# Performance work log

Measured on AMD Instinct MI355X. Metric: run time of the kernel, lower is better.

## Reference

```python
import jax, jax.numpy as jnp
import numpy as np

BS, T, N = 16, 50, 100
OBS, ACT, HID, LAT = 40, 8, 64, 16
NEG = -9e15


def _gat(x, adj, w, a_src, a_dst, b, concat, alpha=0.2):
    # x: [B, n, fin]; w: [H, fin, fout]
    h = jnp.einsum('bni,hio->bhno', x, w)
    e_src = jnp.einsum('bhno,ho->bhn', h, a_src[..., 0])
    e_dst = jnp.einsum('bhno,ho->bhn', h, a_dst[..., 0])
    e = e_src[:, :, :, None] + e_dst[:, :, None, :]        # [B,H,n,n]
    e = jnp.where(e > 0, e, alpha * e)                     # LeakyReLU
    e = jnp.where(adj[None, None] > 0, e, NEG)             # mask by adjacency
    att = jax.nn.softmax(e, axis=-1)
    hp = jnp.einsum('bhnm,bhmo->bhno', att, h)
    if concat:
        B, H, n, fo = hp.shape
        return jax.nn.elu(hp.transpose(0, 2, 1, 3).reshape(B, n, H * fo) + b)
    return hp.mean(axis=1) + b


def _lstm(x, Wih, Whh, bih, bhh):
    # x: [B, T, H]; PyTorch gate order i, f, g, o
    def step(carry, xt):
        h, c = carry
        g = xt @ Wih + h @ Whh + bih + bhh
        i, f, gg, o = jnp.split(g, 4, axis=-1)
        c = jax.nn.sigmoid(f) * c + jax.nn.sigmoid(i) * jnp.tanh(gg)
        h = jax.nn.sigmoid(o) * jnp.tanh(c)
        return (h, c), h
    h0 = jnp.zeros((x.shape[0], Whh.shape[0]), x.dtype)
    _, ys = jax.lax.scan(step, (h0, h0), x.transpose(1, 0, 2))
    return ys.transpose(1, 0, 2)


def _forward(o, a_prev, m, eps, params, adj):
    (W_obs, b_obs, W_pa, b_pa, W_mk, b_mk, id_emb,
     lWih, lWhh, lbih, lbhh,
     e1w, e1s, e1d, e1b, e2w, e2s, e2d, e2b,
     d1w, d1s, d1d, d1b, d2w, d2s, d2d, d2b,
     d3w, d3s, d3d, d3b) = params
    bs, t, n, _ = o.shape
    # encode: summed embeddings (dropout is identity in eval)
    emb = (o @ W_obs + b_obs) + (a_prev @ W_pa + b_pa) + (m @ W_mk + b_mk) + id_emb[None, None]
    x = emb.transpose(0, 2, 1, 3).reshape(bs * n, t, HID)
    x = _lstm(x, lWih, lWhh, lbih, lbhh)
    x = x.reshape(bs, n, t, HID).transpose(0, 2, 1, 3).reshape(bs * t, n, HID)
    x = _gat(x, adj, e1w, e1s, e1d, e1b, True)
    x = _gat(x, adj, e2w, e2s, e2d, e2b, False)
    logits = x.reshape(bs, t, n, 2 * LAT).mean(axis=-2)    # AverageGlobalPool over nodes
    mu, logvar = jnp.split(logits, 2, axis=-1)
    z = mu + eps * jnp.exp(0.5 * logvar)                   # reparameterize
    zu = jnp.repeat(z[:, :, None, :], n, axis=2)           # RepeatGlobalUnpool
    d = jnp.concatenate([emb, zu], axis=-1).reshape(bs * t, n, HID + LAT)
    d = _gat(d, adj, d1w, d1s, d1d, d1b, True)
    d = _gat(d, adj, d2w, d2s, d2d, d2b, True)
    d = _gat(d, adj, d3w, d3s, d3d, d3b, False)
    a_recon = d.reshape(bs, t, n, ACT) * m
    return a_recon, mu, logvar


def setup_inputs() -> dict:
    key = jax.random.key(0)
    it = iter(jax.random.split(key, 48))
    def nrm(shape, s=0.1):
        return s * jax.random.normal(next(it), shape, jnp.float32)
    inp = {}
    inp['o'] = jax.random.normal(next(it), (BS, T, N, OBS), jnp.float32)
    inp['a_prev'] = jax.random.uniform(next(it), (BS, T, N, ACT), jnp.float32)
    inp['m'] = (jax.random.uniform(next(it), (BS, T, N, ACT)) > 0.5).astype(jnp.float32)
    inp['eps'] = jax.random.normal(next(it), (BS, T, LAT), jnp.float32)
    adj = jax.random.randint(next(it), (N, N), 0, 2).astype(jnp.int32)
    inp['adj'] = adj.at[jnp.arange(N), jnp.arange(N)].set(1)
    inp['W_obs'] = nrm((OBS, HID)); inp['b_obs'] = jnp.zeros((HID,), jnp.float32)
    inp['W_pa'] = nrm((ACT, HID)); inp['b_pa'] = jnp.zeros((HID,), jnp.float32)
    inp['W_mk'] = nrm((ACT, HID)); inp['b_mk'] = jnp.zeros((HID,), jnp.float32)
    inp['id_emb'] = nrm((N, HID), 1.0)
    inp['lWih'] = nrm((HID, 4 * HID)); inp['lWhh'] = nrm((HID, 4 * HID))
    inp['lbih'] = jnp.zeros((4 * HID,), jnp.float32); inp['lbhh'] = jnp.zeros((4 * HID,), jnp.float32)
    def gat_p(pfx, H, fin, fout, bdim):
        inp[pfx + 'w'] = nrm((H, fin, fout))
        inp[pfx + 's'] = nrm((H, fout, 1))
        inp[pfx + 'd'] = nrm((H, fout, 1))
        inp[pfx + 'b'] = jnp.zeros((bdim,), jnp.float32)
    gat_p('e1', 4, HID, HID // 4, HID)
    gat_p('e2', 1, HID, 2 * LAT, 2 * LAT)
    gat_p('d1', 4, LAT + HID, HID // 4, HID)
    gat_p('d2', 4, HID, HID // 4, HID)
    gat_p('d3', 1, HID, ACT, ACT)
    return inp


def reference(o, a_prev, m, eps, adj, W_obs, b_obs, W_pa, b_pa, W_mk, b_mk, id_emb,
              lWih, lWhh, lbih, lbhh,
              e1w, e1s, e1d, e1b, e2w, e2s, e2d, e2b,
              d1w, d1s, d1d, d1b, d2w, d2s, d2d, d2b,
              d3w, d3s, d3d, d3b):
    params = (W_obs, b_obs, W_pa, b_pa, W_mk, b_mk, id_emb,
              lWih, lWhh, lbih, lbhh,
              e1w, e1s, e1d, e1b, e2w, e2s, e2d, e2b,
              d1w, d1s, d1d, d1b, d2w, d2s, d2d, d2b,
              d3w, d3s, d3d, d3b)
    return _forward(o, a_prev, m, eps, params, adj)
```

## Files before the change

kernel.cpp:

```cpp
#include <hip/hip_runtime.h>

#define BS  16
#define TT  50
#define NN  100
#define OBSF 40
#define ACTF 8
#define HIDF 64
#define LATF 16

__device__ __forceinline__ float sigmf(float x) { return 1.f / (1.f + __expf(-x)); }
__device__ __forceinline__ float tanh_fast(float x) { return 1.f - 2.f / (__expf(2.f * x) + 1.f); }

__global__ void adjmask_kernel(const int* __restrict__ adj, unsigned long long* __restrict__ mask) {
    int n = threadIdx.x;
    if (n < NN) {
        unsigned long long w0 = 0ull, w1 = 0ull;
        for (int m = 0; m < 64; ++m)  if (adj[n * NN + m] > 0) w0 |= (1ull << m);
        for (int m = 64; m < NN; ++m) if (adj[n * NN + m] > 0) w1 |= (1ull << (m - 64));
        mask[2 * n] = w0; mask[2 * n + 1] = w1;
    }
}

__global__ void emb_kernel(const float* __restrict__ o, const float* __restrict__ ap,
                           const float* __restrict__ mk,
                           const float* __restrict__ Wobs, const float* __restrict__ bobs,
                           const float* __restrict__ Wpa, const float* __restrict__ bpa,
                           const float* __restrict__ Wmk, const float* __restrict__ bmk,
                           const float* __restrict__ idemb, float* __restrict__ emb) {
    int g = blockIdx.x;
    int n = g % NN;
    int j = threadIdx.x;
    __shared__ float so[OBSF], sa[ACTF], sm[ACTF];
    if (j < OBSF) so[j] = o[(size_t)g * OBSF + j];
    if (j >= 40 && j < 48) sa[j - 40] = ap[(size_t)g * ACTF + (j - 40)];
    if (j >= 48 && j < 56) sm[j - 48] = mk[(size_t)g * ACTF + (j - 48)];
    __syncthreads();
    float acc = bobs[j] + bpa[j] + bmk[j] + idemb[n * HIDF + j];
    #pragma unroll
    for (int k = 0; k < OBSF; ++k) acc += so[k] * Wobs[k * HIDF + j];
    #pragma unroll
    for (int k = 0; k < ACTF; ++k) acc += sa[k] * Wpa[k * HIDF + j] + sm[k] * Wmk[k * HIDF + j];
    emb[(size_t)g * HIDF + j] = acc;
}

__global__ void xw_kernel(const float* __restrict__ emb, const float* __restrict__ Wih,
                          const float* __restrict__ bih, const float* __restrict__ bhh,
                          float* __restrict__ xW) {
    int blk = blockIdx.x;
    int chunk = blk % 5;
    int s = blk / 5;
    int b = s / NN, n = s % NN;
    int t0 = chunk * 10;
    __shared__ float se[10][HIDF];
    int tid = threadIdx.x;
    for (int i = tid; i < 10 * HIDF; i += 256) {
        int r = i >> 6, k = i & 63;
        se[r][k] = emb[((size_t)(b * TT + t0 + r) * NN + n) * HIDF + k];
    }
    __syncthreads();
    int j = tid;
    float base = bih[j] + bhh[j];
    float acc[10];
    #pragma unroll
    for (int r = 0; r < 10; ++r) acc[r] = base;
    for (int k = 0; k < HIDF; ++k) {
        float w = Wih[k * 256 + j];
        #pragma unroll
        for (int r = 0; r < 10; ++r) acc[r] += se[r][k] * w;
    }
    #pragma unroll
    for (int r = 0; r < 10; ++r) xW[((size_t)s * TT + t0 + r) * 256 + j] = acc[r];
}

__launch_bounds__(256)
__global__ void lstm_kernel(const float* __restrict__ xW, const float* __restrict__ Whh,
                            float* __restrict__ xenc) {
    int s = blockIdx.x;
    int b = s / NN, n = s % NN;
    int j = threadIdx.x;
    __shared__ __align__(16) float hs[HIDF];
    __shared__ float gs[256];
    float wcol[HIDF];
    #pragma unroll
    for (int k = 0; k < HIDF; ++k) wcol[k] = Whh[k * 256 + j];
    if (j < HIDF) hs[j] = 0.f;
    float c = 0.f;
    __syncthreads();
    for (int t = 0; t < TT; ++t) {
        float acc = xW[((size_t)s * TT + t) * 256 + j];
        const float4* h4 = (const float4*)hs;
        #pragma unroll
        for (int k4 = 0; k4 < HIDF / 4; ++k4) {
            float4 hv = h4[k4];
            acc += hv.x * wcol[4 * k4] + hv.y * wcol[4 * k4 + 1]
                 + hv.z * wcol[4 * k4 + 2] + hv.w * wcol[4 * k4 + 3];
        }
        gs[j] = acc;
        __syncthreads();
        if (j < HIDF) {
            float ig = sigmf(gs[j]);
            float fg = sigmf(gs[64 + j]);
            float gg = tanh_fast(gs[128 + j]);
            float og = sigmf(gs[192 + j]);
            c = fg * c + ig * gg;
            float h = og * tanh_fast(c);
            hs[j] = h;
            xenc[((size_t)(b * TT + t) * NN + n) * HIDF + j] = h;
        }
        __syncthreads();
    }
}

template <int FIN1, int FIN2, int H, int FOUT, int SPLIT, int OUTMODE>
__launch_bounds__(256)
__global__ void gat_kernel(const float* __restrict__ x1, const float* __restrict__ x2,
                           const float* __restrict__ w, const float* __restrict__ asrc,
                           const float* __restrict__ adst, const float* __restrict__ bias,
                           const unsigned long long* __restrict__ adjmask,
                           const float* __restrict__ mgate, float* __restrict__ out) {
    constexpr int FIN = FIN1 + FIN2;
    constexpr int HF = H * FOUT;
    constexpr int NPT = 256 / HF;
    constexpr int ROWS = (NN + NPT - 1) / NPT;
    constexpr int SB = NN * (FIN > HF ? FIN : HF);
    __shared__ __align__(16) float sbuf[SB];
    __shared__ __align__(16) float ses[H * NN];
    __shared__ __align__(16) float sed[H * NN];
    __shared__ unsigned long long smask[2 * NN];
    int g = blockIdx.x;
    int tid = threadIdx.x;

    for (int i = tid; i < NN * FIN1; i += 256) {
        int n = i / FIN1, k = i % FIN1;
        sbuf[n * FIN + k] = x1[((size_t)g * NN + n) * FIN1 + k];
    }
    if constexpr (FIN2 > 0) {
        for (int i = tid; i < NN * FIN2; i += 256) {
            int n = i / FIN2, k = i % FIN2;
            sbuf[n * FIN + FIN1 + k] = x2[(size_t)g * FIN2 + k];
        }
    }
    if (tid < 2 * NN) smask[tid] = adjmask[tid];
    __syncthreads();

    const int ho = tid % HF;
    const int h = ho / FOUT, o = ho % FOUT;
    const int n0 = tid / HF;
    float racc[ROWS];
    {
        float wcol[FIN];
        #pragma unroll
        for (int k = 0; k < FIN; ++k) wcol[k] = w[(h * FIN + k) * FOUT + o];
        const float as = asrc[ho], ad = adst[ho];
        #pragma unroll
        for (int r = 0; r < ROWS; ++r) {
            int n = n0 + r * NPT;
            float acc = 0.f;
            if (ROWS * NPT == NN || n < NN) {
                const float4* row = (const float4*)&sbuf[n * FIN];
                #pragma unroll
                for (int k4 = 0; k4 < FIN / 4; ++k4) {
                    float4 xv = row[k4];
                    acc += xv.x * wcol[4 * k4] + xv.y * wcol[4 * k4 + 1]
                         + xv.z * wcol[4 * k4 + 2] + xv.w * wcol[4 * k4 + 3];
                }
            }
            racc[r] = acc;
            float vs = acc * as, vd = acc * ad;
            #pragma unroll
            for (int off = FOUT / 2; off >= 1; off >>= 1) {
                vs += __shfl_xor(vs, off, 64);
                vd += __shfl_xor(vd, off, 64);
            }
            if (o == 0 && (ROWS * NPT == NN || n < NN)) {
                ses[h * NN + n] = vs; sed[h * NN + n] = vd;
            }
        }
    }
    __syncthreads();
    #pragma unroll
    for (int r = 0; r < ROWS; ++r) {
        int n = n0 + r * NPT;
        if (ROWS * NPT == NN || n < NN) sbuf[n * HF + ho] = racc[r];
    }
    __syncthreads();

    constexpr int FT = FOUT / SPLIT;
    constexpr int ITEMS = H * NN * SPLIT;
    for (int idx = tid; idx < ITEMS; idx += 256) {
        int h2 = idx / (NN * SPLIT);
        int rem = idx % (NN * SPLIT);
        int n = rem / SPLIT;
        int os = (rem % SPLIT) * FT;
        unsigned long long m0 = smask[2 * n], m1 = smask[2 * n + 1];
        float esn = ses[h2 * NN + n];
        float denom = 0.f;
        float acc[FT];
        #pragma unroll
        for (int q = 0; q < FT; ++q) acc[q] = 0.f;
        const float4* sed4 = (const float4*)&sed[h2 * NN];
        #pragma unroll 2
        for (int g4 = 0; g4 < NN / 4; ++g4) {
            float4 ev = sed4[g4];
            unsigned int bits = (g4 < 16) ? (unsigned int)(m0 >> (4 * g4))
                                          : (unsigned int)(m1 >> (4 * g4 - 64));
            float e0 = esn + ev.x; e0 = (e0 > 0.f) ? e0 : 0.2f * e0;
            float e1 = esn + ev.y; e1 = (e1 > 0.f) ? e1 : 0.2f * e1;
            float e2 = esn + ev.z; e2 = (e2 > 0.f) ? e2 : 0.2f * e2;
            float e3 = esn + ev.w; e3 = (e3 > 0.f) ? e3 : 0.2f * e3;
            float p0 = (bits & 1u) ? __expf(e0) : 0.f;
            float p1 = (bits & 2u) ? __expf(e1) : 0.f;
            float p2 = (bits & 4u) ? __expf(e2) : 0.f;
            float p3 = (bits & 8u) ? __expf(e3) : 0.f;
            denom += (p0 + p1) + (p2 + p3);
            const float* r0 = &sbuf[(4 * g4 + 0) * HF + h2 * FOUT + os];
            const float* r1 = &sbuf[(4 * g4 + 1) * HF + h2 * FOUT + os];
            const float* r2 = &sbuf[(4 * g4 + 2) * HF + h2 * FOUT + os];
            const float* r3 = &sbuf[(4 * g4 + 3) * HF + h2 * FOUT + os];
            #pragma unroll
            for (int q4 = 0; q4 < FT / 4; ++q4) {
                float4 v0 = ((const float4*)r0)[q4];
                float4 v1 = ((const float4*)r1)[q4];
                float4 v2 = ((const float4*)r2)[q4];
                float4 v3 = ((const float4*)r3)[q4];
                acc[4 * q4 + 0] += p0 * v0.x + p1 * v1.x + p2 * v2.x + p3 * v3.x;
                acc[4 * q4 + 1] += p0 * v0.y + p1 * v1.y + p2 * v2.y + p3 * v3.y;
                acc[4 * q4 + 2] += p0 * v0.z + p1 * v1.z + p2 * v2.z + p3 * v3.z;
                acc[4 * q4 + 3] += p0 * v0.w + p1 * v1.w + p2 * v2.w + p3 * v3.w;
            }
        }
        float inv = 1.f / denom;
        if constexpr (OUTMODE == 0) {
            float4* op = (float4*)&out[((size_t)g * NN + n) * HF + h2 * FOUT + os];
            #pragma unroll
            for (int q4 = 0; q4 < FT / 4; ++q4) {
                float4 v;
                float a0 = acc[4 * q4 + 0] * inv + bias[h2 * FOUT + os + 4 * q4 + 0];
                float a1 = acc[4 * q4 + 1] * inv + bias[h2 * FOUT + os + 4 * q4 + 1];
                float a2 = acc[4 * q4 + 2] * inv + bias[h2 * FOUT + os + 4 * q4 + 2];
                float a3 = acc[4 * q4 + 3] * inv + bias[h2 * FOUT + os + 4 * q4 + 3];
                v.x = (a0 > 0.f) ? a0 : (__expf(a0) - 1.f);
                v.y = (a1 > 0.f) ? a1 : (__expf(a1) - 1.f);
                v.z = (a2 > 0.f) ? a2 : (__expf(a2) - 1.f);
                v.w = (a3 > 0.f) ? a3 : (__expf(a3) - 1.f);
                op[q4] = v;
            }
        } else if constexpr (OUTMODE == 1) {
            float4* op = (float4*)&out[((size_t)g * NN + n) * FOUT + os];
            #pragma unroll
            for (int q4 = 0; q4 < FT / 4; ++q4) {
                float4 v;
                v.x = acc[4 * q4 + 0] * inv + bias[os + 4 * q4 + 0];
                v.y = acc[4 * q4 + 1] * inv + bias[os + 4 * q4 + 1];
                v.z = acc[4 * q4 + 2] * inv + bias[os + 4 * q4 + 2];
                v.w = acc[4 * q4 + 3] * inv + bias[os + 4 * q4 + 3];
                op[q4] = v;
            }
        } else {
            size_t base = ((size_t)g * NN + n) * FOUT + os;
            float4* op = (float4*)&out[base];
            const float4* mp = (const float4*)&mgate[base];
            #pragma unroll
            for (int q4 = 0; q4 < FT / 4; ++q4) {
                float4 mv = mp[q4];
                float4 v;
                v.x = (acc[4 * q4 + 0] * inv + bias[os + 4 * q4 + 0]) * mv.x;
                v.y = (acc[4 * q4 + 1] * inv + bias[os + 4 * q4 + 1]) * mv.y;
                v.z = (acc[4 * q4 + 2] * inv + bias[os + 4 * q4 + 2]) * mv.z;
                v.w = (acc[4 * q4 + 3] * inv + bias[os + 4 * q4 + 3]) * mv.w;
                op[q4] = v;
            }
        }
    }
}

__global__ void pool_kernel(const float* __restrict__ g2, const float* __restrict__ eps,
                            float* __restrict__ z, float* __restrict__ dout) {
    int g = blockIdx.x;
    int c = threadIdx.x;
    __shared__ float s[2 * LATF];
    if (c < 2 * LATF) {
        float sum = 0.f;
        for (int n = 0; n < NN; ++n) sum += g2[((size_t)g * NN + n) * (2 * LATF) + c];
        s[c] = sum * (1.f / NN);
    }
    __syncthreads();
    if (c < LATF) {
        float mu = s[c], lv = s[LATF + c];
        dout[640000 + (size_t)g * LATF + c] = mu;
        dout[652800 + (size_t)g * LATF + c] = lv;
        z[(size_t)g * LATF + c] = mu + eps[(size_t)g * LATF + c] * __expf(0.5f * lv);
    }
}

extern "C" void kernel_launch(void* const* d_in, const int* in_sizes, int n_in,
                              void* d_out, int out_size, void* d_ws, size_t ws_size,
                              hipStream_t stream) {
    const float* o     = (const float*)d_in[0];
    const float* aprev = (const float*)d_in[1];
    const float* mk    = (const float*)d_in[2];
    const float* eps   = (const float*)d_in[3];
    const int*   adj   = (const int*)d_in[4];
    const float* Wobs  = (const float*)d_in[5];
    const float* bobs  = (const float*)d_in[6];
    const float* Wpa   = (const float*)d_in[7];
    const float* bpa   = (const float*)d_in[8];
    const float* Wmk   = (const float*)d_in[9];
    const float* bmk   = (const float*)d_in[10];
    const float* idemb = (const float*)d_in[11];
    const float* lWih  = (const float*)d_in[12];
    const float* lWhh  = (const float*)d_in[13];
    const float* lbih  = (const float*)d_in[14];
    const float* lbhh  = (const float*)d_in[15];
    const float* e1w = (const float*)d_in[16]; const float* e1s = (const float*)d_in[17];
    const float* e1d = (const float*)d_in[18]; const float* e1b = (const float*)d_in[19];
    const float* e2w = (const float*)d_in[20]; const float* e2s = (const float*)d_in[21];
    const float* e2d = (const float*)d_in[22]; const float* e2b = (const float*)d_in[23];
    const float* d1w = (const float*)d_in[24]; const float* d1s = (const float*)d_in[25];
    const float* d1d = (const float*)d_in[26]; const float* d1b = (const float*)d_in[27];
    const float* d2w = (const float*)d_in[28]; const float* d2s = (const float*)d_in[29];
    const float* d2d = (const float*)d_in[30]; const float* d2b = (const float*)d_in[31];
    const float* d3w = (const float*)d_in[32]; const float* d3s = (const float*)d_in[33];
    const float* d3d = (const float*)d_in[34]; const float* d3b = (const float*)d_in[35];

    float* ws   = (float*)d_ws;
    float* emb  = ws;
    float* xenc = ws + 5120000;
    float* xW   = ws + 10240000;
    float* g1o  = ws + 10240000;
    float* g2o  = ws + 15360000;
    float* z    = ws + 17920000;
    float* d1o  = ws + 18000000;
    float* d2o  = ws + 23200000;
    unsigned long long* amask = (unsigned long long*)(ws + 30720000);
    float* out = (float*)d_out;

    adjmask_kernel<<<1, 128, 0, stream>>>(adj, amask);
    emb_kernel<<<BS * TT * NN, 64, 0, stream>>>(o, aprev, mk, Wobs, bobs, Wpa, bpa,
                                                Wmk, bmk, idemb, emb);
    xw_kernel<<<1600 * 5, 256, 0, stream>>>(emb, lWih, lbih, lbhh, xW);
    lstm_kernel<<<1600, 256, 0, stream>>>(xW, lWhh, xenc);
    gat_kernel<64, 0, 4, 16, 1, 0><<<800, 256, 0, stream>>>(xenc, nullptr, e1w, e1s, e1d, e1b,
                                                            amask, nullptr, g1o);
    gat_kernel<64, 0, 1, 32, 4, 1><<<800, 256, 0, stream>>>(g1o, nullptr, e2w, e2s, e2d, e2b,
                                                            amask, nullptr, g2o);
    pool_kernel<<<800, 64, 0, stream>>>(g2o, eps, z, out);
    gat_kernel<64, 16, 4, 16, 1, 0><<<800, 256, 0, stream>>>(emb, z, d1w, d1s, d1d, d1b,
                                                             amask, nullptr, d1o);
    gat_kernel<64, 0, 4, 16, 1, 0><<<800, 256, 0, stream>>>(d1o, nullptr, d2w, d2s, d2d, d2b,
                                                            amask, nullptr, d2o);
    gat_kernel<64, 0, 1, 8, 2, 2><<<800, 256, 0, stream>>>(d2o, nullptr, d3w, d3s, d3d, d3b,
                                                           amask, mk, out);
}
```

Baseline: 590.8 us.

## Run 4-head GAT layers on bf16 MFMA for projection and attention aggregation

Adds a new GAT kernel for the three 4-head layers. It computes the feature projection and the attention-weighted aggregation with 16x16x32 bf16 MFMA instructions instead of scalar FP32 loops. Attention weights are packed to bf16, and the softmax denominator is accumulated from the truncated values so it stays consistent with them. The adjacency mask is also stored as 32-bit words. This trades bf16 precision in the projections and attention weights for matrix-core throughput.

```diff
diff --git a/kernel.cpp b/kernel.cpp
--- a/kernel.cpp
+++ b/kernel.cpp
@@ -8,16 +8,45 @@
 #define HIDF 64
 #define LATF 16
 
+typedef __attribute__((ext_vector_type(8))) short bf16x8;
+typedef __attribute__((ext_vector_type(4))) float f32x4;
+
 __device__ __forceinline__ float sigmf(float x) { return 1.f / (1.f + __expf(-x)); }
 __device__ __forceinline__ float tanh_fast(float x) { return 1.f - 2.f / (__expf(2.f * x) + 1.f); }
 
-__global__ void adjmask_kernel(const int* __restrict__ adj, unsigned long long* __restrict__ mask) {
+__device__ __forceinline__ unsigned bf16pk_rne(float a, float b) {
+    unsigned ua = __float_as_uint(a); ua += 0x7fffu + ((ua >> 16) & 1u);
+    unsigned ub = __float_as_uint(b); ub += 0x7fffu + ((ub >> 16) & 1u);
+    return (ua >> 16) | (ub & 0xffff0000u);
+}
+__device__ __forceinline__ unsigned bf16pk_trunc(float a, float b) {
+    return (__float_as_uint(a) >> 16) | (__float_as_uint(b) & 0xffff0000u);
+}
+__device__ __forceinline__ float bf16trunc_f(float a) {
+    return __uint_as_float(__float_as_uint(a) & 0xffff0000u);
+}
+
+__global__ void adjmask_kernel(const int* __restrict__ adj, unsigned long long* __restrict__ mask,
+                               unsigned* __restrict__ mask32) {
     int n = threadIdx.x;
-    if (n < NN) {
-        unsigned long long w0 = 0ull, w1 = 0ull;
-        for (int m = 0; m < 64; ++m)  if (adj[n * NN + m] > 0) w0 |= (1ull << m);
-        for (int m = 64; m < NN; ++m) if (adj[n * NN + m] > 0) w1 |= (1ull << (m - 64));
-        mask[2 * n] = w0; mask[2 * n + 1] = w1;
+    if (n < 112) {
+        unsigned d0 = 0, d1 = 0, d2 = 0, d3 = 0;
+        if (n < NN) {
+            for (int m = 0; m < NN; ++m) {
+                if (adj[n * NN + m] > 0) {
+                    if (m < 32) d0 |= 1u << m;
+                    else if (m < 64) d1 |= 1u << (m - 32);
+                    else if (m < 96) d2 |= 1u << (m - 64);
+                    else d3 |= 1u << (m - 96);
+                }
+            }
+        }
+        mask32[n * 4 + 0] = d0; mask32[n * 4 + 1] = d1;
+        mask32[n * 4 + 2] = d2; mask32[n * 4 + 3] = d3;
+        if (n < NN) {
+            mask[2 * n] = (unsigned long long)d0 | ((unsigned long long)d1 << 32);
+            mask[2 * n + 1] = (unsigned long long)d2 | ((unsigned long long)d3 << 32);
+        }
     }
 }
 
@@ -108,6 +137,179 @@
             xenc[((size_t)(b * TT + t) * NN + n) * HIDF + j] = h;
         }
         __syncthreads();
+    }
+}
+
+template <int FIN1, int FIN2>
+__launch_bounds__(256)
+__global__ void gat4_mfma_kernel(const float* __restrict__ x1, const float* __restrict__ x2,
+                                 const float* __restrict__ w, const float* __restrict__ asrc,
+                                 const float* __restrict__ adst, const float* __restrict__ bias,
+                                 const unsigned* __restrict__ mask32, float* __restrict__ out) {
+    constexpr int FIN = FIN1 + FIN2;
+    constexpr int FINP = (FIN + 31) & ~31;
+    constexpr int KC1 = FINP / 32;
+    constexpr int SXP = FINP + 8;
+    constexpr int SWP = FINP + 8;
+    constexpr int SH2P = 136;
+    constexpr int R1A = 112 * SXP * 2;
+    constexpr int R1B = 4 * 16 * SH2P * 2;
+    constexpr int R1 = (R1A > R1B) ? R1A : R1B;
+    constexpr int R2A = 64 * SWP * 2;
+    constexpr int R2B = (448 + 512 + 448 + 448) * 4;
+    constexpr int R2 = (R2A > R2B) ? R2A : R2B;
+    __shared__ __align__(16) char smem[R1 + R2];
+    short* sxa = (short*)smem;
+    short* sh2 = (short*)smem;
+    short* swb = (short*)(smem + R1);
+    float* ses = (float*)(smem + R1);
+    float* sed = ses + 448;
+    float* sden = sed + 512;
+    unsigned* smk = (unsigned*)(sden + 448);
+
+    const int g = blockIdx.x, tid = threadIdx.x;
+    const int wv = tid >> 6, lane = tid & 63, q = lane >> 4, c = lane & 15;
+    const int head = wv;
+
+    for (int i = tid; i < 112 * (SXP / 2); i += 256) {
+        int n = i / (SXP / 2), k2 = i % (SXP / 2);
+        int k = 2 * k2;
+        float lo = 0.f, hi = 0.f;
+        if (n < NN) {
+            if (k < FIN1) {
+                float2 v = *(const float2*)&x1[((size_t)g * NN + n) * FIN1 + k];
+                lo = v.x; hi = v.y;
+            } else if (FIN2 > 0 && k < FIN) {
+                float2 v = *(const float2*)&x2[(size_t)g * FIN2 + (k - FIN1)];
+                lo = v.x; hi = v.y;
+            }
+        }
+        ((unsigned*)sxa)[i] = bf16pk_rne(lo, hi);
+    }
+    for (int i = tid; i < 64 * (SWP / 2); i += 256) {
+        int nc = i / (SWP / 2), k2 = i % (SWP / 2);
+        int h = nc >> 4, o = nc & 15, k = 2 * k2;
+        float lo = 0.f, hi = 0.f;
+        if (k < FIN) {
+            lo = w[((size_t)h * FIN + k) * 16 + o];
+            if (k + 1 < FIN) hi = w[((size_t)h * FIN + k + 1) * 16 + o];
+        }
+        ((unsigned*)swb)[i] = bf16pk_rne(lo, hi);
+    }
+    __syncthreads();
+
+    const float asv = asrc[head * 16 + c], adv = adst[head * 16 + c];
+    const float biasv = bias[head * 16 + c];
+    f32x4 hc[7];
+    #pragma unroll
+    for (int mt = 0; mt < 7; ++mt) hc[mt] = f32x4{0.f, 0.f, 0.f, 0.f};
+    #pragma unroll
+    for (int kc = 0; kc < KC1; ++kc) {
+        bf16x8 bfr = *(const bf16x8*)&swb[(head * 16 + c) * SWP + kc * 32 + q * 8];
+        #pragma unroll
+        for (int mt = 0; mt < 7; ++mt) {
+            bf16x8 afr = *(const bf16x8*)&sxa[(mt * 16 + c) * SXP + kc * 32 + q * 8];
+            hc[mt] = __builtin_amdgcn_mfma_f32_16x16x32_bf16(afr, bfr, hc[mt], 0, 0, 0);
+        }
+    }
+    __syncthreads();
+
+    #pragma unroll
+    for (int mt = 0; mt < 7; ++mt) {
+        float h0 = hc[mt][0], h1 = hc[mt][1], h2 = hc[mt][2], h3 = hc[mt][3];
+        uint2 pk;
+        pk.x = bf16pk_rne(h0, h1);
+        pk.y = bf16pk_rne(h2, h3);
+        *(uint2*)&sh2[(head * 16 + c) * SH2P + mt * 16 + q * 4] = pk;
+        float es0 = h0 * asv, es1 = h1 * asv, es2 = h2 * asv, es3 = h3 * asv;
+        float ed0 = h0 * adv, ed1 = h1 * adv, ed2 = h2 * adv, ed3 = h3 * adv;
+        #pragma unroll
+        for (int off = 1; off <= 8; off <<= 1) {
+            es0 += __shfl_xor(es0, off, 64); es1 += __shfl_xor(es1, off, 64);
+            es2 += __shfl_xor(es2, off, 64); es3 += __shfl_xor(es3, off, 64);
+            ed0 += __shfl_xor(ed0, off, 64); ed1 += __shfl_xor(ed1, off, 64);
+            ed2 += __shfl_xor(ed2, off, 64); ed3 += __shfl_xor(ed3, off, 64);
+        }
+        if (c == 0) {
+            int nb = mt * 16 + q * 4;
+            ses[head * 112 + nb + 0] = es0; ses[head * 112 + nb + 1] = es1;
+            ses[head * 112 + nb + 2] = es2; ses[head * 112 + nb + 3] = es3;
+            sed[head * 128 + nb + 0] = ed0; sed[head * 128 + nb + 1] = ed1;
+            sed[head * 128 + nb + 2] = ed2; sed[head * 128 + nb + 3] = ed3;
+        }
+    }
+    if (lane < 16) {
+        uint4 z4 = {0u, 0u, 0u, 0u};
+        *(uint4*)&sh2[(head * 16 + lane) * SH2P + 112] = z4;
+        *(uint4*)&sh2[(head * 16 + lane) * SH2P + 120] = z4;
+        sed[head * 128 + 112 + lane] = 0.f;
+    }
+    for (int i = tid; i < 448; i += 256) smk[i] = mask32[i];
+    __syncthreads();
+
+    float esr[7];
+    #pragma unroll
+    for (int mt = 0; mt < 7; ++mt) esr[mt] = ses[head * 112 + mt * 16 + c];
+    f32x4 c2[7];
+    float dnp[7];
+    #pragma unroll
+    for (int mt = 0; mt < 7; ++mt) { c2[mt] = f32x4{0.f, 0.f, 0.f, 0.f}; dnp[mt] = 0.f; }
+    #pragma unroll
+    for (int kc = 0; kc < 4; ++kc) {
+        float4 edA = *(const float4*)&sed[head * 128 + kc * 32 + q * 8];
+        float4 edB = *(const float4*)&sed[head * 128 + kc * 32 + q * 8 + 4];
+        bf16x8 bfr = *(const bf16x8*)&sh2[(head * 16 + c) * SH2P + kc * 32 + q * 8];
+        #pragma unroll
+        for (int mt = 0; mt < 7; ++mt) {
+            unsigned mrow = smk[(mt * 16 + c) * 4 + kc];
+            unsigned mb = (mrow >> (q * 8)) & 0xffu;
+            float es = esr[mt];
+            float e0 = es + edA.x; e0 = fmaxf(e0, 0.2f * e0);
+            float e1 = es + edA.y; e1 = fmaxf(e1, 0.2f * e1);
+            float e2 = es + edA.z; e2 = fmaxf(e2, 0.2f * e2);
+            float e3 = es + edA.w; e3 = fmaxf(e3, 0.2f * e3);
+            float e4 = es + edB.x; e4 = fmaxf(e4, 0.2f * e4);
+            float e5 = es + edB.y; e5 = fmaxf(e5, 0.2f * e5);
+            float e6 = es + edB.z; e6 = fmaxf(e6, 0.2f * e6);
+            float e7 = es + edB.w; e7 = fmaxf(e7, 0.2f * e7);
+            float p0 = (mb & 1u)   ? __expf(e0) : 0.f;
+            float p1 = (mb & 2u)   ? __expf(e1) : 0.f;
+            float p2 = (mb & 4u)   ? __expf(e2) : 0.f;
+            float p3 = (mb & 8u)   ? __expf(e3) : 0.f;
+            float p4 = (mb & 16u)  ? __expf(e4) : 0.f;
+            float p5 = (mb & 32u)  ? __expf(e5) : 0.f;
+            float p6 = (mb & 64u)  ? __expf(e6) : 0.f;
+            float p7 = (mb & 128u) ? __expf(e7) : 0.f;
+            union { unsigned u[4]; bf16x8 v; } af;
+            af.u[0] = bf16pk_trunc(p0, p1);
+            af.u[1] = bf16pk_trunc(p2, p3);
+            af.u[2] = bf16pk_trunc(p4, p5);
+            af.u[3] = bf16pk_trunc(p6, p7);
+            dnp[mt] += ((bf16trunc_f(p0) + bf16trunc_f(p1)) + (bf16trunc_f(p2) + bf16trunc_f(p3)))
+                     + ((bf16trunc_f(p4) + bf16trunc_f(p5)) + (bf16trunc_f(p6) + bf16trunc_f(p7)));
+            c2[mt] = __builtin_amdgcn_mfma_f32_16x16x32_bf16(af.v, bfr, c2[mt], 0, 0, 0);
+        }
+    }
+    #pragma unroll
+    for (int mt = 0; mt < 7; ++mt) {
+        float d = dnp[mt];
+        d += __shfl_xor(d, 16, 64);
+        d += __shfl_xor(d, 32, 64);
+        if (q == 0) sden[head * 112 + mt * 16 + c] = d;
+    }
+    #pragma unroll
+    for (int mt = 0; mt < 7; ++mt) {
+        float4 dv = *(const float4*)&sden[head * 112 + mt * 16 + q * 4];
+        float dvr[4] = {dv.x, dv.y, dv.z, dv.w};
+        #pragma unroll
+        for (int r = 0; r < 4; ++r) {
+            int n = mt * 16 + q * 4 + r;
+            if (n < NN) {
+                float v = c2[mt][r] / dvr[r] + biasv;
+                v = (v > 0.f) ? v : (__expf(v) - 1.f);
+                out[((size_t)g * NN + n) * 64 + head * 16 + c] = v;
+            }
+        }
     }
 }
 
@@ -197,7 +399,7 @@
         float denom = 0.f;
         float acc[FT];
         #pragma unroll
-        for (int q = 0; q < FT; ++q) acc[q] = 0.f;
+        for (int qq = 0; qq < FT; ++qq) acc[qq] = 0.f;
         const float4* sed4 = (const float4*)&sed[h2 * NN];
         #pragma unroll 2
         for (int g4 = 0; g4 < NN / 4; ++g4) {
@@ -230,22 +432,7 @@
             }
         }
         float inv = 1.f / denom;
-        if constexpr (OUTMODE == 0) {
-            float4* op = (float4*)&out[((size_t)g * NN + n) * HF + h2 * FOUT + os];
-            #pragma unroll
-            for (int q4 = 0; q4 < FT / 4; ++q4) {
-                float4 v;
-                float a0 = acc[4 * q4 + 0] * inv + bias[h2 * FOUT + os + 4 * q4 + 0];
-                float a1 = acc[4 * q4 + 1] * inv + bias[h2 * FOUT + os + 4 * q4 + 1];
-                float a2 = acc[4 * q4 + 2] * inv + bias[h2 * FOUT + os + 4 * q4 + 2];
-                float a3 = acc[4 * q4 + 3] * inv + bias[h2 * FOUT + os + 4 * q4 + 3];
-                v.x = (a0 > 0.f) ? a0 : (__expf(a0) - 1.f);
-                v.y = (a1 > 0.f) ? a1 : (__expf(a1) - 1.f);
-                v.z = (a2 > 0.f) ? a2 : (__expf(a2) - 1.f);
-                v.w = (a3 > 0.f) ? a3 : (__expf(a3) - 1.f);
-                op[q4] = v;
-            }
-        } else if constexpr (OUTMODE == 1) {
+        if constexpr (OUTMODE == 1) {
             float4* op = (float4*)&out[((size_t)g * NN + n) * FOUT + os];
             #pragma unroll
             for (int q4 = 0; q4 < FT / 4; ++q4) {
@@ -333,22 +520,23 @@
     float* d1o  = ws + 18000000;
     float* d2o  = ws + 23200000;
     unsigned long long* amask = (unsigned long long*)(ws + 30720000);
+    unsigned* mask32 = (unsigned*)(ws + 30720400);
     float* out = (float*)d_out;
 
-    adjmask_kernel<<<1, 128, 0, stream>>>(adj, amask);
+    adjmask_kernel<<<1, 128, 0, stream>>>(adj, amask, mask32);
     emb_kernel<<<BS * TT * NN, 64, 0, stream>>>(o, aprev, mk, Wobs, bobs, Wpa, bpa,
                                                 Wmk, bmk, idemb, emb);
     xw_kernel<<<1600 * 5, 256, 0, stream>>>(emb, lWih, lbih, lbhh, xW);
     lstm_kernel<<<1600, 256, 0, stream>>>(xW, lWhh, xenc);
-    gat_kernel<64, 0, 4, 16, 1, 0><<<800, 256, 0, stream>>>(xenc, nullptr, e1w, e1s, e1d, e1b,
-                                                            amask, nullptr, g1o);
+    gat4_mfma_kernel<64, 0><<<800, 256, 0, stream>>>(xenc, nullptr, e1w, e1s, e1d, e1b,
+                                                     mask32, g1o);
     gat_kernel<64, 0, 1, 32, 4, 1><<<800, 256, 0, stream>>>(g1o, nullptr, e2w, e2s, e2d, e2b,
                                                             amask, nullptr, g2o);
     pool_kernel<<<800, 64, 0, stream>>>(g2o, eps, z, out);
-    gat_kernel<64, 16, 4, 16, 1, 0><<<800, 256, 0, stream>>>(emb, z, d1w, d1s, d1d, d1b,
-                                                             amask, nullptr, d1o);
-    gat_kernel<64, 0, 4, 16, 1, 0><<<800, 256, 0, stream>>>(d1o, nullptr, d2w, d2s, d2d, d2b,
-                                                            amask, nullptr, d2o);
+    gat4_mfma_kernel<64, 16><<<800, 256, 0, stream>>>(emb, z, d1w, d1s, d1d, d1b,
+                                                      mask32, d1o);
+    gat4_mfma_kernel<64, 0><<<800, 256, 0, stream>>>(d1o, nullptr, d2w, d2s, d2d, d2b,
+                                                     mask32, d2o);
     gat_kernel<64, 0, 1, 8, 2, 2><<<800, 256, 0, stream>>>(d2o, nullptr, d3w, d3s, d3d, d3b,
                                                            amask, mk, out);
 }
```

After: 634.4 us. +7.4%, slower.
